# Performance work log

Hardware: AMD Instinct MI355X
Metric: run time of the kernel (lower is better)

The kernel has to match this reference:

```python
import jax, jax.numpy as jnp
import numpy as np

EPS_SINKHORN = 0.01   # entropic regularization (cost / eps)
EPS_LOG = 1e-8        # numerical epsilon inside logs
NUM_ITERS = 50


def setup_inputs() -> dict:
    key = jax.random.key(0)
    k1, k2 = jax.random.split(key)
    B, N = 8, 2048
    x1 = jax.random.normal(k1, (B, N, 3), dtype=jnp.float32)
    x2 = jax.random.normal(k2, (B, N, 3), dtype=jnp.float32)
    return {"x1": x1, "x2": x2}


def reference(x1, x2):
    # x1, x2: [B, N, 3] point clouds
    B, N, _ = x1.shape
    # pairwise squared-distance cost matrix: [B, N, N]
    cost = jnp.sum((x1[:, :, None, :] - x2[:, None, :, :]) ** 2, axis=-1)
    K = jnp.exp(-cost / EPS_SINKHORN)  # constant across iterations

    inv_n = jnp.float32(1.0 / N)
    mu = jnp.full((B, N), inv_n, dtype=cost.dtype)
    nu = jnp.full((B, N), inv_n, dtype=cost.dtype)
    log_mu = jnp.log(mu + EPS_LOG)
    log_nu = jnp.log(nu + EPS_LOG)

    def step(carry, _):
        u, v = carry
        # row update: sum_j K_ij * exp(v_j)
        u = log_mu - jnp.log(jnp.einsum('bij,bj->bi', K, jnp.exp(v)) + EPS_LOG)
        # col update: sum_i K_ij * exp(u_i)
        v = log_nu - jnp.log(jnp.einsum('bij,bi->bj', K, jnp.exp(u)) + EPS_LOG)
        return (u, v), None

    u0 = jnp.zeros((B, N), dtype=cost.dtype)
    v0 = jnp.zeros((B, N), dtype=cost.dtype)
    (u, v), _ = jax.lax.scan(step, (u0, v0), None, length=NUM_ITERS)

    transport = K * jnp.exp(u[:, :, None] + v[:, None, :])  # [B, N, N]
    emd = jnp.sum(transport * cost, axis=(1, 2))            # [B]
    return emd
```

## Files before the change

### kernel.cpp

```cpp
#include <hip/hip_runtime.h>
#include <cmath>

#define BATCH 8
#define NPT   2048
#define NPAIR (NPT / 2)
#define NPTS  (BATCH * NPT)
#define TILES 64
#define GRID_MAIN (BATCH * TILES)
#define THREADS 512
#define ITERS 50

#define C_LOG2E 1.4426950408889634f
#define NEG100C (-144.26950408889634f)
#define S200C   288.53900817779268f
#define EPS_LOG 1e-8f
#define LN2_01  0.006931471805599453f

typedef float v2f __attribute__((ext_vector_type(2)));
typedef float v4f __attribute__((ext_vector_type(4)));
typedef unsigned long long u64t;

static __device__ __forceinline__ float fast_exp2(float x) {
#if __has_builtin(__builtin_amdgcn_exp2f)
    return __builtin_amdgcn_exp2f(x);
#else
    return exp2f(x);
#endif
}

static __device__ __forceinline__ v2f pk_fma(v2f a, v2f b, v2f c) {
    v2f d;
    asm("v_pk_fma_f32 %0, %1, %2, %3" : "=v"(d) : "v"(a), "v"(b), "v"(c));
    return d;
}
static __device__ __forceinline__ v2f pk_add(v2f a, v2f b) {
    v2f d;
    asm("v_pk_add_f32 %0, %1, %2" : "=v"(d) : "v"(a), "v"(b));
    return d;
}

static __device__ __forceinline__ float gload(const float* p) {
    return __hip_atomic_load(p, __ATOMIC_RELAXED, __HIP_MEMORY_SCOPE_AGENT);
}
static __device__ __forceinline__ void gstore(float* p, float val) {
    __hip_atomic_store(p, val, __ATOMIC_RELAXED, __HIP_MEMORY_SCOPE_AGENT);
}
static __device__ __forceinline__ u64t gload2(const float* p) {
    return __hip_atomic_load((const u64t*)p, __ATOMIC_RELAXED,
                             __HIP_MEMORY_SCOPE_AGENT);
}

__global__ void init_kernel(float* __restrict__ out,
                            unsigned int* __restrict__ flags) {
    int t = threadIdx.x;
    if (t < BATCH) out[t] = 0.0f;
    flags[t] = 0u;
}

static __device__ __forceinline__ void flag_barrier(unsigned int* bflags,
                                                    int tile, int wave,
                                                    int lane,
                                                    unsigned int phase) {
    __syncthreads();
    if (wave == 0) {
        if (lane == 0)
            __hip_atomic_store(&bflags[tile], phase, __ATOMIC_RELAXED,
                               __HIP_MEMORY_SCOPE_AGENT);
        while (__hip_atomic_load(&bflags[lane], __ATOMIC_RELAXED,
                                 __HIP_MEMORY_SCOPE_AGENT) < phase) {
            __builtin_amdgcn_s_sleep(1);
        }
    }
    __syncthreads();
    __builtin_amdgcn_sched_barrier(0);
}

static __device__ __forceinline__ void fold_dual(v4f* cdZW, const float* dual,
        int base, int tid, const float (&Pa)[2], const float (&Pb)[2]) {
    u64t d0 = gload2(dual + base + 4 * tid);
    u64t d1 = gload2(dual + base + 4 * tid + 2);
    float a0 = __uint_as_float((unsigned)d0);
    float b0 = __uint_as_float((unsigned)(d0 >> 32));
    float a1 = __uint_as_float((unsigned)d1);
    float b1 = __uint_as_float((unsigned)(d1 >> 32));
    reinterpret_cast<v2f*>(&cdZW[2 * tid])[1] =
        (v2f){fmaf(C_LOG2E, a0, Pa[0]), fmaf(C_LOG2E, b0, Pb[0])};
    reinterpret_cast<v2f*>(&cdZW[2 * tid + 1])[1] =
        (v2f){fmaf(C_LOG2E, a1, Pa[1]), fmaf(C_LOG2E, b1, Pb[1])};
}

static __device__ __forceinline__ float half_core(
        const v4f* cdXY, const v4f* cdZW, int p0,
        v2f RX, v2f RY, v2f RZ, v2f RC)
{
    float accx = 0.0f, accy = 0.0f;
#pragma unroll 4
    for (int s = 0; s < 64; s++) {
        v4f a  = cdXY[p0 + s];
        v4f bz = cdZW[p0 + s];
        v2f xx = __builtin_shufflevector(a,  a,  0, 1);
        v2f yy = __builtin_shufflevector(a,  a,  2, 3);
        v2f zz = __builtin_shufflevector(bz, bz, 0, 1);
        v2f ww = __builtin_shufflevector(bz, bz, 2, 3);
        v2f t = pk_fma(xx, RX, ww);
        t = pk_fma(yy, RY, t);
        t = pk_fma(zz, RZ, t);
        t = pk_add(t, RC);
        accx += fast_exp2(t.x);
        accy += fast_exp2(t.y);
    }
    return accx + accy;
}

__global__ __launch_bounds__(THREADS, 4) void sinkhorn_kernel(
        const float* __restrict__ x1, const float* __restrict__ x2,
        float* __restrict__ u, float* __restrict__ v,
        unsigned int* __restrict__ flags, float* __restrict__ out)
{
    __shared__ v4f cd1XY[NPAIR], cd1ZW[NPAIR];
    __shared__ v4f cd2XY[NPAIR], cd2ZW[NPAIR];
    __shared__ float part[32][9];

    const int b    = blockIdx.x / TILES;
    const int tile = blockIdx.x % TILES;
    const int base = b * NPT;
    unsigned int* bflags = flags + b * TILES;

    const int tid  = threadIdx.x;
    const int wave = tid >> 6;
    const int lane = tid & 63;
    const int rloc = lane & 31;
    const int ch   = lane >> 5;
    const int row  = tile * 32 + rloc;
    const int p0   = wave * 128 + ch * 64;

    const float log_mu = logf(1.0f / (float)NPT + EPS_LOG);

    float P1a[2], P1b[2], P2a[2], P2b[2];
#pragma unroll
    for (int k = 0; k < 2; k++) {
        int q = 2 * tid + k;
        const float* p = x1 + 3 * (base + 2 * q);
        float ax = p[0], ay = p[1], az = p[2];
        float bx = p[3], by = p[4], bz = p[5];
        float na = fmaf(ax, ax, fmaf(ay, ay, az * az));
        float nb = fmaf(bx, bx, fmaf(by, by, bz * bz));
        P1a[k] = na * NEG100C;  P1b[k] = nb * NEG100C;
        cd1XY[q] = (v4f){ax * S200C, bx * S200C, ay * S200C, by * S200C};
        cd1ZW[q] = (v4f){az * S200C, bz * S200C, P1a[k], P1b[k]};

        p = x2 + 3 * (base + 2 * q);
        ax = p[0]; ay = p[1]; az = p[2];
        bx = p[3]; by = p[4]; bz = p[5];
        na = fmaf(ax, ax, fmaf(ay, ay, az * az));
        nb = fmaf(bx, bx, fmaf(by, by, bz * bz));
        P2a[k] = na * NEG100C;  P2b[k] = nb * NEG100C;
        cd2XY[q] = (v4f){ax * S200C, bx * S200C, ay * S200C, by * S200C};
        cd2ZW[q] = (v4f){az * S200C, bz * S200C, P2a[k], P2b[k]};
    }

    v2f RX1, RY1, RZ1, RC1, RX2, RY2, RZ2, RC2;
    float rc1s;
    {
        const float* p = x1 + 3 * (base + row);
        float a = p[0], bb = p[1], c = p[2];
        float nn = NEG100C * fmaf(a, a, fmaf(bb, bb, c * c));
        RX1 = (v2f){a, a};  RY1 = (v2f){bb, bb};
        RZ1 = (v2f){c, c};  RC1 = (v2f){nn, nn};
        rc1s = nn;
        p = x2 + 3 * (base + row);
        a = p[0]; bb = p[1]; c = p[2];
        nn = NEG100C * fmaf(a, a, fmaf(bb, bb, c * c));
        RX2 = (v2f){a, a};  RY2 = (v2f){bb, bb};
        RZ2 = (v2f){c, c};  RC2 = (v2f){nn, nn};
    }
    __syncthreads();

    unsigned int ph = 0;
    for (int it = 0; it < ITERS; it++) {
        if (it > 0) {
            fold_dual(cd2ZW, v, base, tid, P2a, P2b);
            __syncthreads();
        }
        {
            float s = half_core(cd2XY, cd2ZW, p0, RX1, RY1, RZ1, RC1);
            s += __shfl_xor(s, 32, 64);
            if (lane < 32) part[rloc][wave] = s;
            __syncthreads();
            if (wave == 0) {
                float t = 0.0f;
#pragma unroll
                for (int w = 0; w < 8; w++) t += part[rloc][w];
                float res = log_mu - __logf(t + EPS_LOG);
                if (lane < 32) gstore(&u[base + row], res);
            }
        }
        flag_barrier(bflags, tile, wave, lane, ++ph);

        fold_dual(cd1ZW, u, base, tid, P1a, P1b);
        __syncthreads();
        {
            float s = half_core(cd1XY, cd1ZW, p0, RX2, RY2, RZ2, RC2);
            s += __shfl_xor(s, 32, 64);
            if (lane < 32) part[rloc][wave] = s;
            __syncthreads();
            if (wave == 0) {
                float t = 0.0f;
#pragma unroll
                for (int w = 0; w < 8; w++) t += part[rloc][w];
                float res = log_mu - __logf(t + EPS_LOG);
                if (lane < 32) gstore(&v[base + row], res);
            }
        }
        flag_barrier(bflags, tile, wave, lane, ++ph);
    }

    v2f* cvp = reinterpret_cast<v2f*>(cd1XY);
    {
        u64t d0 = gload2(v + base + 4 * tid);
        u64t d1 = gload2(v + base + 4 * tid + 2);
        float a0 = __uint_as_float((unsigned)d0);
        float b0 = __uint_as_float((unsigned)(d0 >> 32));
        float a1 = __uint_as_float((unsigned)d1);
        float b1 = __uint_as_float((unsigned)(d1 >> 32));
        reinterpret_cast<v2f*>(&cd2ZW[2 * tid])[1] =
            (v2f){fmaf(C_LOG2E, a0, P2a[0]), fmaf(C_LOG2E, b0, P2b[0])};
        reinterpret_cast<v2f*>(&cd2ZW[2 * tid + 1])[1] =
            (v2f){fmaf(C_LOG2E, a1, P2a[1]), fmaf(C_LOG2E, b1, P2b[1])};
        cvp[2 * tid]     = (v2f){0.01f * a0, 0.01f * b0};
        cvp[2 * tid + 1] = (v2f){0.01f * a1, 0.01f * b1};
    }
    __syncthreads();

    float ur = gload(&u[base + row]);
    float rcs = fmaf(C_LOG2E, ur, rc1s);
    v2f RCC = (v2f){rcs, rcs};
    float sus = 0.01f * ur;
    v2f SU = (v2f){sus, sus};

    const v2f NL2 = {-LN2_01, -LN2_01};
    v2f eacc = {0.0f, 0.0f};
#pragma unroll 4
    for (int s = 0; s < 64; s++) {
        v4f a   = cd2XY[p0 + s];
        v4f bz  = cd2ZW[p0 + s];
        v2f cv2 = cvp[p0 + s];
        v2f xx = __builtin_shufflevector(a,  a,  0, 1);
        v2f yy = __builtin_shufflevector(a,  a,  2, 3);
        v2f zz = __builtin_shufflevector(bz, bz, 0, 1);
        v2f ww = __builtin_shufflevector(bz, bz, 2, 3);
        v2f t = pk_fma(xx, RX1, ww);
        t = pk_fma(yy, RY1, t);
        t = pk_fma(zz, RZ1, t);
        t = pk_add(t, RCC);
        v2f c2 = pk_fma(t, NL2, pk_add(SU, cv2));
        eacc.x = fmaf(fast_exp2(t.x), c2.x, eacc.x);
        eacc.y = fmaf(fast_exp2(t.y), c2.y, eacc.y);
    }
    float es = eacc.x + eacc.y;
#pragma unroll
    for (int m = 32; m >= 1; m >>= 1) es += __shfl_xor(es, m, 64);

    __syncthreads();
    if (lane == 0) part[0][wave] = es;
    __syncthreads();
    if (tid == 0) {
        float s = 0.0f;
#pragma unroll
        for (int w = 0; w < 8; w++) s += part[0][w];
        atomicAdd(&out[b], s);
    }
}

extern "C" void kernel_launch(void* const* d_in, const int* in_sizes, int n_in,
                              void* d_out, int out_size, void* d_ws, size_t ws_size,
                              hipStream_t stream) {
    (void)in_sizes; (void)n_in; (void)out_size; (void)ws_size;
    const float* x1 = (const float*)d_in[0];
    const float* x2 = (const float*)d_in[1];
    float* out = (float*)d_out;

    char* ws = (char*)d_ws;
    float* u = (float*)ws;
    float* v = u + NPTS;
    unsigned int* flags = (unsigned int*)(v + NPTS);

    init_kernel<<<1, 512, 0, stream>>>(out, flags);
    sinkhorn_kernel<<<GRID_MAIN, THREADS, 0, stream>>>(x1, x2, u, v, flags, out);
}
```

Measured before the change: 813.7 us.

## Replace block-wide barriers with flag polling and shared-signal broadcast in Sinkhorn loop

Restructures the per-iteration grid barrier. Wave 0 now publishes the tile flag with a release store right after writing its dual values, then polls the other tiles' flags and broadcasts completion through a shared-memory signal that the other waves spin on. This removes the __syncthreads calls around the barrier and after each dual fold, replacing them with a local s_waitcnt. The row-partial reduction now uses vectorized LDS reads from a padded array. The goal is to cut intra-block synchronization latency on the 100 serialized half-steps, but waves now read LDS entries folded by other waves without a block barrier, which risks a race.

```diff
diff --git a/kernel.cpp b/kernel.cpp
--- a/kernel.cpp
+++ b/kernel.cpp
@@ -55,38 +55,6 @@
     int t = threadIdx.x;
     if (t < BATCH) out[t] = 0.0f;
     flags[t] = 0u;
-}
-
-static __device__ __forceinline__ void flag_barrier(unsigned int* bflags,
-                                                    int tile, int wave,
-                                                    int lane,
-                                                    unsigned int phase) {
-    __syncthreads();
-    if (wave == 0) {
-        if (lane == 0)
-            __hip_atomic_store(&bflags[tile], phase, __ATOMIC_RELAXED,
-                               __HIP_MEMORY_SCOPE_AGENT);
-        while (__hip_atomic_load(&bflags[lane], __ATOMIC_RELAXED,
-                                 __HIP_MEMORY_SCOPE_AGENT) < phase) {
-            __builtin_amdgcn_s_sleep(1);
-        }
-    }
-    __syncthreads();
-    __builtin_amdgcn_sched_barrier(0);
-}
-
-static __device__ __forceinline__ void fold_dual(v4f* cdZW, const float* dual,
-        int base, int tid, const float (&Pa)[2], const float (&Pb)[2]) {
-    u64t d0 = gload2(dual + base + 4 * tid);
-    u64t d1 = gload2(dual + base + 4 * tid + 2);
-    float a0 = __uint_as_float((unsigned)d0);
-    float b0 = __uint_as_float((unsigned)(d0 >> 32));
-    float a1 = __uint_as_float((unsigned)d1);
-    float b1 = __uint_as_float((unsigned)(d1 >> 32));
-    reinterpret_cast<v2f*>(&cdZW[2 * tid])[1] =
-        (v2f){fmaf(C_LOG2E, a0, Pa[0]), fmaf(C_LOG2E, b0, Pb[0])};
-    reinterpret_cast<v2f*>(&cdZW[2 * tid + 1])[1] =
-        (v2f){fmaf(C_LOG2E, a1, Pa[1]), fmaf(C_LOG2E, b1, Pb[1])};
 }
 
 static __device__ __forceinline__ float half_core(
@@ -119,7 +87,8 @@
 {
     __shared__ v4f cd1XY[NPAIR], cd1ZW[NPAIR];
     __shared__ v4f cd2XY[NPAIR], cd2ZW[NPAIR];
-    __shared__ float part[32][9];
+    __shared__ __align__(16) float part[32][12];
+    __shared__ unsigned int sig;
 
     const int b    = blockIdx.x / TILES;
     const int tile = blockIdx.x % TILES;
@@ -158,6 +127,7 @@
         cd2XY[q] = (v4f){ax * S200C, bx * S200C, ay * S200C, by * S200C};
         cd2ZW[q] = (v4f){az * S200C, bz * S200C, P2a[k], P2b[k]};
     }
+    if (tid == 0) sig = 0u;
 
     v2f RX1, RY1, RZ1, RC1, RX2, RY2, RZ2, RC2;
     float rc1s;
@@ -176,44 +146,71 @@
     }
     __syncthreads();
 
-    unsigned int ph = 0;
-    for (int it = 0; it < ITERS; it++) {
-        if (it > 0) {
-            fold_dual(cd2ZW, v, base, tid, P2a, P2b);
-            __syncthreads();
-        }
-        {
-            float s = half_core(cd2XY, cd2ZW, p0, RX1, RY1, RZ1, RC1);
-            s += __shfl_xor(s, 32, 64);
-            if (lane < 32) part[rloc][wave] = s;
-            __syncthreads();
-            if (wave == 0) {
-                float t = 0.0f;
-#pragma unroll
-                for (int w = 0; w < 8; w++) t += part[rloc][w];
-                float res = log_mu - __logf(t + EPS_LOG);
-                if (lane < 32) gstore(&u[base + row], res);
+    auto waitph = [&](unsigned int ph) {
+        if (wave == 0) {
+            while (__hip_atomic_load(&bflags[lane], __ATOMIC_RELAXED,
+                                     __HIP_MEMORY_SCOPE_AGENT) < ph) {
+                __builtin_amdgcn_s_sleep(1);
+            }
+            if (lane == 0)
+                __hip_atomic_store(&sig, ph, __ATOMIC_RELAXED,
+                                   __HIP_MEMORY_SCOPE_WORKGROUP);
+        } else {
+            while (__hip_atomic_load(&sig, __ATOMIC_RELAXED,
+                                     __HIP_MEMORY_SCOPE_WORKGROUP) < ph) {
+                __builtin_amdgcn_s_sleep(1);
             }
         }
-        flag_barrier(bflags, tile, wave, lane, ++ph);
-
-        fold_dual(cd1ZW, u, base, tid, P1a, P1b);
+        __builtin_amdgcn_sched_barrier(0);
+    };
+    auto fold2 = [&](v4f* ZW, const float* dual,
+                     const float (&Pa)[2], const float (&Pb)[2]) {
+        u64t d0 = gload2(dual + base + 4 * tid);
+        u64t d1 = gload2(dual + base + 4 * tid + 2);
+        reinterpret_cast<v2f*>(&ZW[2 * tid])[1] = (v2f){
+            fmaf(C_LOG2E, __uint_as_float((unsigned)d0), Pa[0]),
+            fmaf(C_LOG2E, __uint_as_float((unsigned)(d0 >> 32)), Pb[0])};
+        reinterpret_cast<v2f*>(&ZW[2 * tid + 1])[1] = (v2f){
+            fmaf(C_LOG2E, __uint_as_float((unsigned)d1), Pa[1]),
+            fmaf(C_LOG2E, __uint_as_float((unsigned)(d1 >> 32)), Pb[1])};
+        asm volatile("s_waitcnt lgkmcnt(0)" ::: "memory");
+    };
+    auto do_phase = [&](const v4f* XY, const v4f* ZW,
+                        v2f RX, v2f RY, v2f RZ, v2f RC,
+                        float* drow, unsigned int php) {
+        float s = half_core(XY, ZW, p0, RX, RY, RZ, RC);
+        s += __shfl_xor(s, 32, 64);
+        if (lane < 32) part[rloc][wave] = s;
         __syncthreads();
-        {
-            float s = half_core(cd1XY, cd1ZW, p0, RX2, RY2, RZ2, RC2);
-            s += __shfl_xor(s, 32, 64);
-            if (lane < 32) part[rloc][wave] = s;
-            __syncthreads();
-            if (wave == 0) {
-                float t = 0.0f;
-#pragma unroll
-                for (int w = 0; w < 8; w++) t += part[rloc][w];
-                float res = log_mu - __logf(t + EPS_LOG);
-                if (lane < 32) gstore(&v[base + row], res);
+        if (wave == 0) {
+            if (lane < 32) {
+                const v4f* pr = reinterpret_cast<const v4f*>(&part[lane][0]);
+                v4f A = pr[0], Bq = pr[1];
+                float t = ((A.x + A.y) + (A.z + A.w)) +
+                          ((Bq.x + Bq.y) + (Bq.z + Bq.w));
+                gstore(drow + lane, log_mu - __logf(t + EPS_LOG));
             }
+            if (lane == 0)
+                __hip_atomic_store(&bflags[tile], php, __ATOMIC_RELEASE,
+                                   __HIP_MEMORY_SCOPE_AGENT);
         }
-        flag_barrier(bflags, tile, wave, lane, ++ph);
-    }
+    };
+
+    float* urow = u + base + tile * 32;
+    float* vrow = v + base + tile * 32;
+
+    do_phase(cd2XY, cd2ZW, RX1, RY1, RZ1, RC1, urow, 1);
+    for (int it = 0; it < ITERS; it++) {
+        waitph(2 * it + 1);
+        fold2(cd1ZW, u, P1a, P1b);
+        do_phase(cd1XY, cd1ZW, RX2, RY2, RZ2, RC2, vrow, 2 * it + 2);
+        if (it < ITERS - 1) {
+            waitph(2 * it + 2);
+            fold2(cd2ZW, v, P2a, P2b);
+            do_phase(cd2XY, cd2ZW, RX1, RY1, RZ1, RC1, urow, 2 * it + 3);
+        }
+    }
+    waitph(2 * ITERS);
 
     v2f* cvp = reinterpret_cast<v2f*>(cd1XY);
     {
@@ -229,8 +226,8 @@
             (v2f){fmaf(C_LOG2E, a1, P2a[1]), fmaf(C_LOG2E, b1, P2b[1])};
         cvp[2 * tid]     = (v2f){0.01f * a0, 0.01f * b0};
         cvp[2 * tid + 1] = (v2f){0.01f * a1, 0.01f * b1};
-    }
-    __syncthreads();
+        asm volatile("s_waitcnt lgkmcnt(0)" ::: "memory");
+    }
 
     float ur = gload(&u[base + row]);
     float rcs = fmaf(C_LOG2E, ur, rc1s);
@@ -261,7 +258,6 @@
 #pragma unroll
     for (int m = 32; m >= 1; m >>= 1) es += __shfl_xor(es, m, 64);
 
-    __syncthreads();
     if (lane == 0) part[0][wave] = es;
     __syncthreads();
     if (tid == 0) {
```

Result: slower. 1.104 ms (+35.7%).
